# Performance work log

Measured on AMD Instinct MI355X. Metric: run time of the kernel, lower is better.

## Reference

```python
import jax, jax.numpy as jnp
import numpy as np

L, B, S, E, H = 6, 8, 1024, 768, 12
D = E // H          # 64, head dim
F = 4 * E           # 3072, FFN hidden
SCALE = np.float32(1.0 / np.sqrt(D))


def setup_inputs() -> dict:
    key = jax.random.key(0)
    ks = jax.random.split(key, 8)
    std = 0.02
    w = lambda k, shape: jax.random.normal(k, shape, jnp.float32) * std
    return {
        "x": jax.random.normal(ks[0], (B, S, E), jnp.float32),
        # per-layer stacked params, leading dim = L
        "ln1_g": jnp.ones((L, E), jnp.float32),
        "ln1_b": jnp.zeros((L, E), jnp.float32),
        "wq": w(ks[1], (L, E, E)),
        "wk": w(ks[2], (L, E, E)),
        "wv": w(ks[3], (L, E, E)),
        "wo_w": w(ks[4], (L, E, E)),
        "wo_b": jnp.zeros((L, E), jnp.float32),
        "ln2_g": jnp.ones((L, E), jnp.float32),
        "ln2_b": jnp.zeros((L, E), jnp.float32),
        "w1_w": w(ks[5], (L, E, F)),
        "w1_b": jnp.zeros((L, F), jnp.float32),
        "w2_w": w(ks[6], (L, F, E)),
        "w2_b": jnp.zeros((L, E), jnp.float32),
    }


def _ln(x, g, b):
    m = jnp.mean(x, axis=-1, keepdims=True)
    v = jnp.var(x, axis=-1, keepdims=True)
    return (x - m) * jax.lax.rsqrt(v + 1e-5) * g + b


def _block(x, p):
    (ln1_g, ln1_b, wq, wk, wv, wo_w, wo_b,
     ln2_g, ln2_b, w1_w, w1_b, w2_w, w2_b) = p
    # pre-LN MHA (same LN applied to q,k,v since q=k=v=x)
    h = _ln(x, ln1_g, ln1_b)
    q = (h @ wq).reshape(B, S, H, D)
    k = (h @ wk).reshape(B, S, H, D)
    v = (h @ wv).reshape(B, S, H, D)
    att = jax.nn.softmax(jnp.einsum('bqhd,bkhd->bhqk', q, k) * SCALE, axis=-1)
    o = jnp.einsum('bhqk,bkhd->bqhd', att, v).reshape(B, S, E)
    x = x + (o @ wo_w + wo_b)
    # pre-LN GELU FFN (torch GELU default = exact erf)
    h = _ln(x, ln2_g, ln2_b)
    x = x + (jax.nn.gelu(h @ w1_w + w1_b, approximate=False) @ w2_w + w2_b)
    return x


def reference(x, ln1_g, ln1_b, wq, wk, wv, wo_w, wo_b,
              ln2_g, ln2_b, w1_w, w1_b, w2_w, w2_b):
    params = (ln1_g, ln1_b, wq, wk, wv, wo_w, wo_b,
              ln2_g, ln2_b, w1_w, w1_b, w2_w, w2_b)

    def step(carry, p):
        return _block(carry, p), None

    out, _ = jax.lax.scan(step, x, params)
    return out
```

## Files before the change

kernel.cpp:

```cpp
#include <hip/hip_runtime.h>
#include <hip/hip_bf16.h>
#include <math.h>

#define L_LAYERS 6
#define B_ 8
#define S_ 1024
#define E_ 768
#define H_ 12
#define D_ 64
#define F_ 3072
#define RSQKV 2304

typedef __bf16 bf16_t;
typedef __bf16 bf16x8 __attribute__((ext_vector_type(8)));
typedef __bf16 bf16x4 __attribute__((ext_vector_type(4)));
typedef float f32x4 __attribute__((ext_vector_type(4)));
typedef unsigned int u32;

__device__ __forceinline__ f32x4 f32x4_zero() {
    f32x4 v; v[0] = 0.f; v[1] = 0.f; v[2] = 0.f; v[3] = 0.f; return v;
}

__device__ __forceinline__ f32x4 mfma16(bf16x8 a, bf16x8 b, f32x4 c) {
    return __builtin_amdgcn_mfma_f32_16x16x32_bf16(a, b, c, 0, 0, 0);
}

__device__ __forceinline__ void gload16(const void* g, void* l) {
    __builtin_amdgcn_global_load_lds((__attribute__((address_space(1))) u32*)g,
                                     (__attribute__((address_space(3))) u32*)l,
                                     16, 0, 0);
}

__global__ __launch_bounds__(256) void wconvT(const float* __restrict__ in,
                                              bf16_t* __restrict__ out,
                                              int K, int N,
                                              size_t outLayerStride, int outRowOff) {
    const size_t lo = (size_t)blockIdx.z * K * N;
    const size_t oo = (size_t)blockIdx.z * outLayerStride;
    const int n0 = blockIdx.x * 64, k0 = blockIdx.y * 64;
    __shared__ float tile[64][65];
    const int t = threadIdx.x;
    {
        const int kr = t >> 4, nq = (t & 15) * 4;
#pragma unroll
        for (int r = 0; r < 4; r++) {
            const float4 vv = *(const float4*)&in[lo + (size_t)(k0 + kr + r * 16) * N + n0 + nq];
            tile[kr + r * 16][nq + 0] = vv.x;
            tile[kr + r * 16][nq + 1] = vv.y;
            tile[kr + r * 16][nq + 2] = vv.z;
            tile[kr + r * 16][nq + 3] = vv.w;
        }
    }
    __syncthreads();
    {
        const int nr = t >> 4, kq = (t & 15) * 4;
#pragma unroll
        for (int r = 0; r < 4; r++) {
            bf16x4 o4;
#pragma unroll
            for (int j = 0; j < 4; j++) o4[j] = (bf16_t)tile[kq + j][nr + r * 16];
            *(bf16x4*)&out[oo + (size_t)(outRowOff + n0 + nr + r * 16) * K + k0 + kq] = o4;
        }
    }
}

__global__ __launch_bounds__(256) void vtransT(const bf16_t* __restrict__ v,
                                               bf16_t* __restrict__ vt) {
    const int s0 = blockIdx.x * 64;
    const int bh = blockIdx.y;
    const int b = bh / H_, h = bh % H_;
    __shared__ bf16_t tile[64][65];
    const int t = threadIdx.x;
    {
        const int si = t >> 2, dq = (t & 3) * 16;
        const bf16_t* src = v + ((size_t)(b * S_ + s0 + si)) * RSQKV + h * D_ + dq;
        bf16x8 a0 = *(const bf16x8*)src;
        bf16x8 a1 = *(const bf16x8*)(src + 8);
#pragma unroll
        for (int j = 0; j < 8; j++) { tile[si][dq + j] = a0[j]; tile[si][dq + 8 + j] = a1[j]; }
    }
    __syncthreads();
    {
        const int di = t >> 2, sq = (t & 3) * 16;
        bf16_t* dst = vt + ((size_t)bh * D_ + di) * S_ + s0 + sq;
        bf16x8 o0, o1;
#pragma unroll
        for (int j = 0; j < 8; j++) { o0[j] = tile[sq + j][di]; o1[j] = tile[sq + 8 + j][di]; }
        *(bf16x8*)dst = o0;
        *(bf16x8*)(dst + 8) = o1;
    }
}

__global__ __launch_bounds__(256) void ln_cast(const float* __restrict__ x,
                                               const float* __restrict__ gamma,
                                               const float* __restrict__ beta,
                                               bf16_t* __restrict__ out) {
    const int row = blockIdx.x;
    const int t = threadIdx.x;
    const float* xr = x + (size_t)row * E_;
    float v0 = xr[t], v1 = xr[t + 256], v2 = xr[t + 512];
    float s = v0 + v1 + v2;
    float sq = v0 * v0 + v1 * v1 + v2 * v2;
#pragma unroll
    for (int off = 32; off >= 1; off >>= 1) {
        s += __shfl_down(s, off);
        sq += __shfl_down(sq, off);
    }
    __shared__ float ps[4], pq[4];
    const int w = t >> 6, lane = t & 63;
    if (lane == 0) { ps[w] = s; pq[w] = sq; }
    __syncthreads();
    s = ps[0] + ps[1] + ps[2] + ps[3];
    sq = pq[0] + pq[1] + pq[2] + pq[3];
    const float mean = s * (1.f / E_);
    const float var = sq * (1.f / E_) - mean * mean;
    const float rstd = rsqrtf(var + 1e-5f);
    bf16_t* orow = out + (size_t)row * E_;
    orow[t] = (bf16_t)((v0 - mean) * rstd * gamma[t] + beta[t]);
    orow[t + 256] = (bf16_t)((v1 - mean) * rstd * gamma[t + 256] + beta[t + 256]);
    orow[t + 512] = (bf16_t)((v2 - mean) * rstd * gamma[t + 512] + beta[t + 512]);
}

template <int EPI>
__global__ __launch_bounds__(256) void gemm_bt(const bf16_t* __restrict__ A,
                                               const bf16_t* __restrict__ BT,
                                               const float* __restrict__ bias,
                                               float* __restrict__ Cf,
                                               bf16_t* __restrict__ Cb,
                                               int M, int N, int K) {
    __shared__ bf16_t Als[128 * 32];
    __shared__ bf16_t Bls[128 * 32];
    const int t = threadIdx.x;
    const int lane = t & 63;
    const int w = t >> 6;
    const int wr = w >> 1, wc = w & 1;
    const int g = lane >> 4, cc = lane & 15;
    const int nwg = gridDim.x * gridDim.y;
    const int lin = blockIdx.y * gridDim.x + blockIdx.x;
    const int swz = (lin & 7) * (nwg >> 3) + (lin >> 3);
    const size_t row0 = (size_t)(swz & 63) * 128;
    const size_t col0 = (size_t)(swz >> 6) * 128;

    f32x4 acc[4][4];
#pragma unroll
    for (int i = 0; i < 4; i++)
#pragma unroll
        for (int j = 0; j < 4; j++) acc[i][j] = f32x4_zero();

    for (int k0 = 0; k0 < K; k0 += 32) {
#pragma unroll
        for (int i = 0; i < 2; i++) {
            const int chunk = i * 256 + t;
            const int ldsbase = (i * 256 + (t & ~63)) * 8;
            gload16(A + (row0 + (chunk >> 2)) * K + k0 + (chunk & 3) * 8, &Als[ldsbase]);
            gload16(BT + (col0 + (chunk >> 2)) * K + k0 + (chunk & 3) * 8, &Bls[ldsbase]);
        }
        __syncthreads();
        bf16x8 af[4], bfr[4];
#pragma unroll
        for (int mi = 0; mi < 4; mi++)
            af[mi] = *(const bf16x8*)&Als[(wr * 64 + mi * 16 + cc) * 32 + g * 8];
#pragma unroll
        for (int ni = 0; ni < 4; ni++)
            bfr[ni] = *(const bf16x8*)&Bls[(wc * 64 + ni * 16 + cc) * 32 + g * 8];
#pragma unroll
        for (int mi = 0; mi < 4; mi++)
#pragma unroll
            for (int ni = 0; ni < 4; ni++)
                acc[mi][ni] = mfma16(af[mi], bfr[ni], acc[mi][ni]);
        __syncthreads();
    }

#pragma unroll
    for (int mi = 0; mi < 4; mi++) {
#pragma unroll
        for (int ni = 0; ni < 4; ni++) {
            const size_t r = row0 + wr * 64 + mi * 16 + g * 4;
            const size_t col = col0 + wc * 64 + ni * 16 + cc;
#pragma unroll
            for (int reg = 0; reg < 4; reg++) {
                const size_t idx = (r + reg) * N + col;
                const float v = acc[mi][ni][reg];
                if (EPI == 1) {
                    Cf[idx] = Cf[idx] + v + bias[col];
                } else if (EPI == 2) {
                    const float xv = v + bias[col];
                    Cb[idx] = (bf16_t)(0.5f * xv * (1.f + erff(xv * 0.70710678118654752440f)));
                } else {
                    Cb[idx] = (bf16_t)(col < 768 ? v * 0.125f : v);
                }
            }
        }
    }
}

__global__ __launch_bounds__(256) void attn_fwd(const bf16_t* __restrict__ Q,
                                                const bf16_t* __restrict__ K,
                                                const bf16_t* __restrict__ VT,
                                                bf16_t* __restrict__ O) {
    const int t = threadIdx.x, lane = t & 63, w = t >> 6;
    const int g = lane >> 4, cc = lane & 15;
    const int hid = blockIdx.x;
    const int logical = (hid & 7) * 96 + (hid >> 3);
    const int qt = logical & 7;
    const int bh = logical >> 3;
    const int b = bh / H_, h = bh % H_;
    const int q0w = qt * 128 + w * 32;
    const size_t qbase = (size_t)b * S_ * RSQKV + h * D_;
    const size_t vtbase = (size_t)bh * D_ * S_;
    const size_t obase = (size_t)b * S_ * E_ + h * D_;

    __shared__ bf16_t Kls[2][64 * 64];
    __shared__ bf16_t Vls[2][64 * 64];
    __shared__ bf16_t Pl[4][32 * 72];

    const int srow = t >> 3;
    const int sslot = (t & 7) ^ (srow & 7);
    const int srow1 = srow + 32;
    const int sslot1 = (t & 7) ^ (srow1 & 7);
    const int ldsb0 = (t & ~63) * 8;
    const int ldsb1 = (256 + (t & ~63)) * 8;

    bf16x8 qf[2][2];
#pragma unroll
    for (int qr = 0; qr < 2; qr++)
#pragma unroll
        for (int kh = 0; kh < 2; kh++)
            qf[qr][kh] = *(const bf16x8*)(Q + qbase + (size_t)(q0w + qr * 16 + cc) * RSQKV + kh * 32 + g * 8);

    f32x4 o_acc[2][4];
#pragma unroll
    for (int qr = 0; qr < 2; qr++)
#pragma unroll
        for (int df = 0; df < 4; df++) o_acc[qr][df] = f32x4_zero();
    float rs_acc[2][4];
#pragma unroll
    for (int qr = 0; qr < 2; qr++)
#pragma unroll
        for (int i = 0; i < 4; i++) rs_acc[qr][i] = 0.f;

#define STAGE_KV(bufi, k0v)                                                                   \
    do {                                                                                      \
        gload16(K + qbase + (size_t)((k0v) + srow) * RSQKV + sslot * 8, &Kls[bufi][ldsb0]);   \
        gload16(K + qbase + (size_t)((k0v) + srow1) * RSQKV + sslot1 * 8, &Kls[bufi][ldsb1]); \
        gload16(VT + vtbase + (size_t)srow * S_ + (k0v) + sslot * 8, &Vls[bufi][ldsb0]);      \
        gload16(VT + vtbase + (size_t)srow1 * S_ + (k0v) + sslot1 * 8, &Vls[bufi][ldsb1]);    \
    } while (0)

    STAGE_KV(0, 0);
    int buf = 0;
    for (int kt = 0; kt < S_ / 64; kt++) {
        if (kt + 1 < S_ / 64) {
            STAGE_KV(buf ^ 1, (kt + 1) * 64);
            asm volatile("s_waitcnt vmcnt(4)" ::: "memory");
        } else {
            asm volatile("s_waitcnt vmcnt(0)" ::: "memory");
        }
        __builtin_amdgcn_s_barrier();
        __builtin_amdgcn_sched_barrier(0);

#pragma unroll
        for (int qr = 0; qr < 2; qr++) {
            f32x4 sc[4];
#pragma unroll
            for (int nf = 0; nf < 4; nf++) sc[nf] = f32x4_zero();
#pragma unroll
            for (int nf = 0; nf < 4; nf++) {
#pragma unroll
                for (int kh = 0; kh < 2; kh++) {
                    bf16x8 kf = *(const bf16x8*)&Kls[buf][(nf * 16 + cc) * 64 + (((kh << 2) + g) ^ (cc & 7)) * 8];
                    sc[nf] = mfma16(qf[qr][kh], kf, sc[nf]);
                }
            }
#pragma unroll
            for (int nf = 0; nf < 4; nf++)
#pragma unroll
                for (int i = 0; i < 4; i++) {
                    const float p = __expf(sc[nf][i]);
                    sc[nf][i] = p;
                    rs_acc[qr][i] += p;
                }
#pragma unroll
            for (int nf = 0; nf < 4; nf++)
#pragma unroll
                for (int i = 0; i < 4; i++)
                    Pl[w][(qr * 16 + g * 4 + i) * 72 + nf * 16 + cc] = (bf16_t)sc[nf][i];
        }
        asm volatile("s_waitcnt lgkmcnt(0)" ::: "memory");
        __builtin_amdgcn_sched_barrier(0);
        bf16x8 pf[2][2];
#pragma unroll
        for (int qr = 0; qr < 2; qr++)
#pragma unroll
            for (int kh = 0; kh < 2; kh++)
                pf[qr][kh] = *(const bf16x8*)&Pl[w][(qr * 16 + cc) * 72 + kh * 32 + g * 8];
#pragma unroll
        for (int df = 0; df < 4; df++) {
#pragma unroll
            for (int kh = 0; kh < 2; kh++) {
                bf16x8 vf = *(const bf16x8*)&Vls[buf][(df * 16 + cc) * 64 + (((kh << 2) + g) ^ (cc & 7)) * 8];
#pragma unroll
                for (int qr = 0; qr < 2; qr++)
                    o_acc[qr][df] = mfma16(pf[qr][kh], vf, o_acc[qr][df]);
            }
        }
        __builtin_amdgcn_s_barrier();
        buf ^= 1;
    }
#undef STAGE_KV

#pragma unroll
    for (int off = 1; off < 16; off <<= 1)
#pragma unroll
        for (int qr = 0; qr < 2; qr++)
#pragma unroll
            for (int i = 0; i < 4; i++) rs_acc[qr][i] += __shfl_xor(rs_acc[qr][i], off);
#pragma unroll
    for (int qr = 0; qr < 2; qr++)
#pragma unroll
        for (int i = 0; i < 4; i++) rs_acc[qr][i] = 1.f / rs_acc[qr][i];
#pragma unroll
    for (int qr = 0; qr < 2; qr++)
#pragma unroll
        for (int df = 0; df < 4; df++)
#pragma unroll
            for (int i = 0; i < 4; i++)
                O[obase + (size_t)(q0w + qr * 16 + g * 4 + i) * E_ + df * 16 + cc] =
                    (bf16_t)(o_acc[qr][df][i] * rs_acc[qr][i]);
}

extern "C" void kernel_launch(void* const* d_in, const int* in_sizes, int n_in,
                              void* d_out, int out_size, void* d_ws, size_t ws_size,
                              hipStream_t stream) {
    const float* x = (const float*)d_in[0];
    const float* ln1_g = (const float*)d_in[1];
    const float* ln1_b = (const float*)d_in[2];
    const float* wq = (const float*)d_in[3];
    const float* wk = (const float*)d_in[4];
    const float* wv = (const float*)d_in[5];
    const float* wo_w = (const float*)d_in[6];
    const float* wo_b = (const float*)d_in[7];
    const float* ln2_g = (const float*)d_in[8];
    const float* ln2_b = (const float*)d_in[9];
    const float* w1_w = (const float*)d_in[10];
    const float* w1_b = (const float*)d_in[11];
    const float* w2_w = (const float*)d_in[12];
    const float* w2_b = (const float*)d_in[13];
    float* xout = (float*)d_out;

    char* ws = (char*)d_ws;
    size_t off = 0;
    auto alloc = [&](size_t bytes) {
        void* p = ws + off;
        off += (bytes + 255) & ~(size_t)255;
        return p;
    };
    const size_t BSE = (size_t)B_ * S_ * E_;
    const size_t qkvLS = (size_t)RSQKV * E_;
    bf16_t* wqkvT = (bf16_t*)alloc((size_t)L_LAYERS * qkvLS * 2);
    bf16_t* woT = (bf16_t*)alloc((size_t)L_LAYERS * E_ * E_ * 2);
    bf16_t* w1T = (bf16_t*)alloc((size_t)L_LAYERS * E_ * F_ * 2);
    bf16_t* w2T = (bf16_t*)alloc((size_t)L_LAYERS * E_ * F_ * 2);
    bf16_t* hbuf = (bf16_t*)alloc(BSE * 2);
    bf16_t* qkvb = (bf16_t*)alloc((size_t)B_ * S_ * F_ * 2);
    bf16_t* ffh = qkvb;
    bf16_t* vtb = (bf16_t*)alloc(BSE * 2);

    dim3 blk(256);
    wconvT<<<dim3(12, 12, 6), blk, 0, stream>>>(wq, wqkvT, E_, E_, qkvLS, 0);
    wconvT<<<dim3(12, 12, 6), blk, 0, stream>>>(wk, wqkvT, E_, E_, qkvLS, 768);
    wconvT<<<dim3(12, 12, 6), blk, 0, stream>>>(wv, wqkvT, E_, E_, qkvLS, 1536);
    wconvT<<<dim3(12, 12, 6), blk, 0, stream>>>(wo_w, woT, E_, E_, (size_t)E_ * E_, 0);
    wconvT<<<dim3(48, 12, 6), blk, 0, stream>>>(w1_w, w1T, E_, F_, (size_t)E_ * F_, 0);
    wconvT<<<dim3(12, 48, 6), blk, 0, stream>>>(w2_w, w2T, F_, E_, (size_t)E_ * F_, 0);
    hipMemcpyAsync(xout, x, BSE * sizeof(float), hipMemcpyDeviceToDevice, stream);

    const int M = B_ * S_;
    for (int l = 0; l < L_LAYERS; l++) {
        const size_t wEE = (size_t)l * E_ * E_;
        const size_t wEF = (size_t)l * E_ * F_;
        ln_cast<<<M, blk, 0, stream>>>(xout, ln1_g + l * E_, ln1_b + l * E_, hbuf);
        gemm_bt<3><<<dim3(64, 18), blk, 0, stream>>>(hbuf, wqkvT + l * qkvLS, nullptr, nullptr, qkvb, M, RSQKV, E_);
        vtransT<<<dim3(16, 96), blk, 0, stream>>>(qkvb + 1536, vtb);
        attn_fwd<<<dim3(768), blk, 0, stream>>>(qkvb, qkvb + 768, vtb, hbuf);
        gemm_bt<1><<<dim3(64, 6), blk, 0, stream>>>(hbuf, woT + wEE, wo_b + l * E_, xout, nullptr, M, E_, E_);
        ln_cast<<<M, blk, 0, stream>>>(xout, ln2_g + l * E_, ln2_b + l * E_, hbuf);
        gemm_bt<2><<<dim3(64, 24), blk, 0, stream>>>(hbuf, w1T + wEF, w1_b + l * F_, nullptr, ffh, M, F_, E_);
        gemm_bt<1><<<dim3(64, 6), blk, 0, stream>>>(ffh, w2T + wEF, w2_b + l * E_, xout, nullptr, M, E_, F_);
    }
}
```

Baseline: 2.293 ms.

## Triple-buffer GEMM LDS loads, add BN=64 tiles for N=768 GEMMs, remap XCD swizzle

The GEMM becomes a 3-stage LDS pipeline. Global loads for tile k+2 are issued before computing tile k, gated by explicit vmcnt waits and raw s_barriers instead of __syncthreads. A BN template parameter lets the two N=768 GEMMs use 128x64 tiles, which doubles their block count from 384 to 768 for better CU occupancy on the narrow outputs. The block-to-tile mapping now uses a 1D grid with XCD-aware row grouping. The cost is three times the LDS and hand-tuned waitcnt values that depend on exact load counts.

```diff
diff --git a/kernel.cpp b/kernel.cpp
--- a/kernel.cpp
+++ b/kernel.cpp
@@ -121,73 +121,98 @@
     orow[t + 512] = (bf16_t)((v2 - mean) * rstd * gamma[t + 512] + beta[t + 512]);
 }
 
-template <int EPI>
+template <int EPI, int BN>
 __global__ __launch_bounds__(256) void gemm_bt(const bf16_t* __restrict__ A,
                                                const bf16_t* __restrict__ BT,
                                                const float* __restrict__ bias,
                                                float* __restrict__ Cf,
                                                bf16_t* __restrict__ Cb,
                                                int M, int N, int K) {
-    __shared__ bf16_t Als[128 * 32];
-    __shared__ bf16_t Bls[128 * 32];
+    constexpr int NF = BN / 32;
+    constexpr int BISS = BN / 64;
+    __shared__ bf16_t Als[3][128 * 32];
+    __shared__ bf16_t Bls[3][BN * 32];
     const int t = threadIdx.x;
     const int lane = t & 63;
     const int w = t >> 6;
     const int wr = w >> 1, wc = w & 1;
     const int g = lane >> 4, cc = lane & 15;
-    const int nwg = gridDim.x * gridDim.y;
-    const int lin = blockIdx.y * gridDim.x + blockIdx.x;
-    const int swz = (lin & 7) * (nwg >> 3) + (lin >> 3);
-    const size_t row0 = (size_t)(swz & 63) * 128;
-    const size_t col0 = (size_t)(swz >> 6) * 128;
-
-    f32x4 acc[4][4];
+    const int ny = N / BN;
+    const int xcd = blockIdx.x & 7, idx = blockIdx.x >> 3;
+    const int colb = idx % ny, rowloc = idx / ny;
+    const size_t row0 = (size_t)(xcd * 8 + rowloc) * 128;
+    const size_t col0 = (size_t)colb * BN;
+
+    f32x4 acc[4][NF];
 #pragma unroll
     for (int i = 0; i < 4; i++)
 #pragma unroll
-        for (int j = 0; j < 4; j++) acc[i][j] = f32x4_zero();
-
-    for (int k0 = 0; k0 < K; k0 += 32) {
-#pragma unroll
-        for (int i = 0; i < 2; i++) {
-            const int chunk = i * 256 + t;
-            const int ldsbase = (i * 256 + (t & ~63)) * 8;
-            gload16(A + (row0 + (chunk >> 2)) * K + k0 + (chunk & 3) * 8, &Als[ldsbase]);
-            gload16(BT + (col0 + (chunk >> 2)) * K + k0 + (chunk & 3) * 8, &Bls[ldsbase]);
-        }
-        __syncthreads();
-        bf16x8 af[4], bfr[4];
+        for (int j = 0; j < NF; j++) acc[i][j] = f32x4_zero();
+
+    const int srow = t >> 2;
+    const int sk = (t & 3) * 8;
+    const int ldsb0 = (t & ~63) * 8;
+    const int ldsb1 = (256 + (t & ~63)) * 8;
+
+    auto GSTAGE = [&](int bi, int k0v) {
+        gload16(A + (row0 + srow) * K + k0v + sk, &Als[bi][ldsb0]);
+        gload16(A + (row0 + 64 + srow) * K + k0v + sk, &Als[bi][ldsb1]);
+        gload16(BT + (col0 + srow) * K + k0v + sk, &Bls[bi][ldsb0]);
+        if constexpr (BISS == 2)
+            gload16(BT + (col0 + 64 + srow) * K + k0v + sk, &Bls[bi][ldsb1]);
+    };
+
+    const int nk = K / 32;
+    GSTAGE(0, 0);
+    GSTAGE(1, 32);
+    int bi = 0, si = 2;
+    for (int kt = 0; kt < nk; kt++) {
+        if (kt + 2 < nk) {
+            GSTAGE(si, (kt + 2) * 32);
+            if constexpr (BN == 128) asm volatile("s_waitcnt vmcnt(8)" ::: "memory");
+            else                     asm volatile("s_waitcnt vmcnt(6)" ::: "memory");
+        } else if (kt + 1 < nk) {
+            if constexpr (BN == 128) asm volatile("s_waitcnt vmcnt(4)" ::: "memory");
+            else                     asm volatile("s_waitcnt vmcnt(3)" ::: "memory");
+        } else {
+            asm volatile("s_waitcnt vmcnt(0)" ::: "memory");
+        }
+        __builtin_amdgcn_s_barrier();
+        __builtin_amdgcn_sched_barrier(0);
+        bf16x8 af[4], bfr[NF];
 #pragma unroll
         for (int mi = 0; mi < 4; mi++)
-            af[mi] = *(const bf16x8*)&Als[(wr * 64 + mi * 16 + cc) * 32 + g * 8];
-#pragma unroll
-        for (int ni = 0; ni < 4; ni++)
-            bfr[ni] = *(const bf16x8*)&Bls[(wc * 64 + ni * 16 + cc) * 32 + g * 8];
+            af[mi] = *(const bf16x8*)&Als[bi][(wr * 64 + mi * 16 + cc) * 32 + g * 8];
+#pragma unroll
+        for (int ni = 0; ni < NF; ni++)
+            bfr[ni] = *(const bf16x8*)&Bls[bi][(wc * (BN / 2) + ni * 16 + cc) * 32 + g * 8];
 #pragma unroll
         for (int mi = 0; mi < 4; mi++)
 #pragma unroll
-            for (int ni = 0; ni < 4; ni++)
+            for (int ni = 0; ni < NF; ni++)
                 acc[mi][ni] = mfma16(af[mi], bfr[ni], acc[mi][ni]);
-        __syncthreads();
+        __builtin_amdgcn_s_barrier();
+        bi = (bi == 2) ? 0 : bi + 1;
+        si = (si == 2) ? 0 : si + 1;
     }
 
 #pragma unroll
     for (int mi = 0; mi < 4; mi++) {
 #pragma unroll
-        for (int ni = 0; ni < 4; ni++) {
+        for (int ni = 0; ni < NF; ni++) {
             const size_t r = row0 + wr * 64 + mi * 16 + g * 4;
-            const size_t col = col0 + wc * 64 + ni * 16 + cc;
+            const size_t col = col0 + wc * (BN / 2) + ni * 16 + cc;
 #pragma unroll
             for (int reg = 0; reg < 4; reg++) {
-                const size_t idx = (r + reg) * N + col;
+                const size_t idx2 = (r + reg) * N + col;
                 const float v = acc[mi][ni][reg];
                 if (EPI == 1) {
-                    Cf[idx] = Cf[idx] + v + bias[col];
+                    Cf[idx2] = Cf[idx2] + v + bias[col];
                 } else if (EPI == 2) {
                     const float xv = v + bias[col];
-                    Cb[idx] = (bf16_t)(0.5f * xv * (1.f + erff(xv * 0.70710678118654752440f)));
+                    Cb[idx2] = (bf16_t)(0.5f * xv * (1.f + erff(xv * 0.70710678118654752440f)));
                 } else {
-                    Cb[idx] = (bf16_t)(col < 768 ? v * 0.125f : v);
+                    Cb[idx2] = (bf16_t)(col < 768 ? v * 0.125f : v);
                 }
             }
         }
@@ -380,12 +405,12 @@
         const size_t wEE = (size_t)l * E_ * E_;
         const size_t wEF = (size_t)l * E_ * F_;
         ln_cast<<<M, blk, 0, stream>>>(xout, ln1_g + l * E_, ln1_b + l * E_, hbuf);
-        gemm_bt<3><<<dim3(64, 18), blk, 0, stream>>>(hbuf, wqkvT + l * qkvLS, nullptr, nullptr, qkvb, M, RSQKV, E_);
+        gemm_bt<3, 128><<<dim3(64 * 18), blk, 0, stream>>>(hbuf, wqkvT + l * qkvLS, nullptr, nullptr, qkvb, M, RSQKV, E_);
         vtransT<<<dim3(16, 96), blk, 0, stream>>>(qkvb + 1536, vtb);
         attn_fwd<<<dim3(768), blk, 0, stream>>>(qkvb, qkvb + 768, vtb, hbuf);
-        gemm_bt<1><<<dim3(64, 6), blk, 0, stream>>>(hbuf, woT + wEE, wo_b + l * E_, xout, nullptr, M, E_, E_);
+        gemm_bt<1, 64><<<dim3(64 * 12), blk, 0, stream>>>(hbuf, woT + wEE, wo_b + l * E_, xout, nullptr, M, E_, E_);
         ln_cast<<<M, blk, 0, stream>>>(xout, ln2_g + l * E_, ln2_b + l * E_, hbuf);
-        gemm_bt<2><<<dim3(64, 24), blk, 0, stream>>>(hbuf, w1T + wEF, w1_b + l * F_, nullptr, ffh, M, F_, E_);
-        gemm_bt<1><<<dim3(64, 6), blk, 0, stream>>>(ffh, w2T + wEF, w2_b + l * E_, xout, nullptr, M, E_, F_);
-    }
-}
+        gemm_bt<2, 128><<<dim3(64 * 24), blk, 0, stream>>>(hbuf, w1T + wEF, w1_b + l * F_, nullptr, ffh, M, F_, E_);
+        gemm_bt<1, 64><<<dim3(64 * 12), blk, 0, stream>>>(ffh, w2T + wEF, w2_b + l * E_, xout, nullptr, M, E_, F_);
+    }
+}
```

Measured after the change: 1.954 ms. 1.17x faster.
